# Optimization experiments

Measured on AMD Instinct MI355X. Metric: run time of the kernel, lower is better.

Reference implementation:

```python
import jax
import jax.numpy as jnp
from jax import lax
import numpy as np

INPUT_DIM = 784
HIDDEN_DIM = 1024
BATCH = 256
N_BINS = 10


def setup_inputs() -> dict:
    key = jax.random.key(0)
    k1, k2, k3, k4, k5 = jax.random.split(key, 5)
    # kaiming-normal-ish init scales (faithful in spirit; exact values irrelevant for math)
    W = jax.random.normal(k1, (HIDDEN_DIM, INPUT_DIM), dtype=jnp.float32) * np.sqrt(2.0 / INPUT_DIM)
    c = jnp.zeros((HIDDEN_DIM, 1), dtype=jnp.float32)
    V = jax.random.normal(k2, (INPUT_DIM, HIDDEN_DIM, N_BINS), dtype=jnp.float32) * np.sqrt(2.0 / N_BINS)
    b = jnp.zeros((INPUT_DIM, N_BINS), dtype=jnp.float32)
    x = jax.random.randint(k3, (BATCH, INPUT_DIM), 0, N_BINS, dtype=jnp.int32)
    return {"x": x, "W": W, "c": c, "V": V, "b": b}


def reference(x, W, c, V, b):
    # x: [B, D] int pixel bins; W: [H, D]; c: [H, 1]; V: [D, H, 10]; b: [D, 10]
    B = x.shape[0]
    xf = x.astype(jnp.float32)  # [B, D]
    a0 = jnp.broadcast_to(c[:, 0][None, :], (B, W.shape[0]))  # [B, H]

    def step(a, inp):
        Vi, bi, Wi, xi = inp  # Vi:[H,10], bi:[10], Wi:[H], xi:[B]
        h = jax.nn.sigmoid(a)                       # [B, H]
        p = jax.nn.softmax(h @ Vi + bi, axis=1)     # [B, 10]
        a = a + xi[:, None] * Wi[None, :]           # rank-1 update, matches x_i @ W[:,i].T
        return a, p

    _, p_seq = lax.scan(step, a0, (V, b, W.T, xf.T))  # p_seq: [D, B, 10]
    p_hat = jnp.transpose(p_seq, (1, 2, 0))            # [B, 10, D] == torch.stack(p_hat, dim=2)
    return p_hat
```

## Files before the change

### kernel.cpp

```cpp
#include <hip/hip_runtime.h>
#include <stdint.h>

#define D_DIM 784
#define H_DIM 1024
#define B_DIM 256
#define NBIN  10
#define G_CH  16
#define T_CH  49
#define BT    16
#define LOG2E 1.4426950408889634f

typedef _Float16 half8_t  __attribute__((ext_vector_type(8)));
typedef __fp16   fp16x2_t __attribute__((ext_vector_type(2)));
typedef float    float4_t __attribute__((ext_vector_type(4)));

__global__ void k_transpose(const float* __restrict__ W, float* __restrict__ Wt2) {
    int j = blockIdx.x;
    int t = threadIdx.x;
    int h = t * 4;
    float4 v;
    v.x = W[(size_t)(h+0)*D_DIM + j] * LOG2E;
    v.y = W[(size_t)(h+1)*D_DIM + j] * LOG2E;
    v.z = W[(size_t)(h+2)*D_DIM + j] * LOG2E;
    v.w = W[(size_t)(h+3)*D_DIM + j] * LOG2E;
    ((float4*)(Wt2 + (size_t)j*H_DIM))[t] = v;
}

__global__ void k_vbprep(const float* __restrict__ V, _Float16* __restrict__ VB) {
    int i  = blockIdx.x;
    int kk = blockIdx.y;
    int t  = threadIdx.x;
    int l  = t >> 1;
    int j0 = (t & 1) * 4;
    int n  = l & 15;
    int hbase = kk*32 + (l>>4)*8 + j0;
    union { _Float16 h[4]; uint2 u; } o;
    #pragma unroll
    for (int jj = 0; jj < 4; ++jj) {
        float v = (n < NBIN) ? V[((size_t)i*H_DIM + hbase + jj)*NBIN + n] : 0.0f;
        o.h[jj] = (_Float16)v;
    }
    size_t idx = ((size_t)(i*32 + kk)*64 + l)*8 + j0;
    *((uint2*)(VB + idx)) = o.u;
}

template<typename CT>
__global__ void k_partial(const float* __restrict__ Wt2, const int* __restrict__ x,
                          CT* __restrict__ PA) {
    int tc   = blockIdx.x;
    int hblk = blockIdx.y;
    int bblk = blockIdx.z;
    int t    = threadIdx.x;
    int h    = hblk*256 + t;

    __shared__ __align__(16) float xs[64][G_CH];
    {
        int bl = t >> 2, q = t & 3;
        int4 xi = *((const int4*)(x + (size_t)(bblk*64 + bl)*D_DIM + tc*G_CH + q*4));
        float4 xf = make_float4((float)xi.x, (float)xi.y, (float)xi.z, (float)xi.w);
        *((float4*)&xs[bl][q*4]) = xf;
    }
    float w[G_CH];
    #pragma unroll
    for (int j = 0; j < G_CH; ++j) w[j] = Wt2[(size_t)(tc*G_CH + j)*H_DIM + h];
    __syncthreads();

    for (int bl = 0; bl < 64; ++bl) {
        float acc = 0.0f;
        #pragma unroll
        for (int q = 0; q < 4; ++q) {
            float4 xf = *((float4*)&xs[bl][q*4]);
            acc += xf.x*w[q*4+0] + xf.y*w[q*4+1] + xf.z*w[q*4+2] + xf.w*w[q*4+3];
        }
        PA[((size_t)tc*B_DIM + bblk*64 + bl)*H_DIM + h] = (CT)acc;
    }
}

template<typename CT>
__global__ void k_scan(const float* __restrict__ c, CT* __restrict__ PA) {
    int b = blockIdx.x >> 2;
    int h = (blockIdx.x & 3)*256 + threadIdx.x;
    float acc = c[h] * LOG2E;
    size_t stride = (size_t)B_DIM * H_DIM;
    size_t idx = (size_t)b*H_DIM + h;
    for (int tt = 0; tt < T_CH; ++tt) {
        float v = (float)PA[idx];
        PA[idx] = (CT)acc;
        acc += v;
        idx += stride;
    }
}

template<typename CT>
__global__ __launch_bounds__(256, 3)
void k_main(const float* __restrict__ Wt2, const _Float16* __restrict__ VB,
            const CT* __restrict__ PA, const int* __restrict__ x,
            const float* __restrict__ bias, float* __restrict__ out) {
    int tc  = blockIdx.x;
    int bt  = blockIdx.y;
    int tid = threadIdx.x;
    int w   = tid >> 6;
    int l   = tid & 63;
    int bl  = l & 15;
    int kg  = l >> 4;
    int bg  = bt*BT + bl;
    int i0  = tc*G_CH;

    __shared__ float red[4][256][5];
    __shared__ float bs[G_CH][16];
    __shared__ __align__(16) float plds[BT][NBIN][20];

    {
        int ii = tid >> 4, n = tid & 15;
        bs[ii][n] = (n < NBIN) ? bias[(size_t)(i0+ii)*NBIN + n] : 0.0f;
    }

    float a[8][8];
    {
        const CT* src = PA + ((size_t)tc*B_DIM + bg)*H_DIM + w*256 + kg*8;
        #pragma unroll
        for (int m = 0; m < 8; ++m)
            #pragma unroll
            for (int j = 0; j < 8; ++j)
                a[m][j] = (float)src[m*32 + j];
    }
    __syncthreads();

    const float4* wt4 = (const float4*)Wt2;
    for (int ii = 0; ii < G_CH; ++ii) {
        int i = i0 + ii;
        float xvf = (float)x[(size_t)bg*D_DIM + i];

        uint4 vb[8];
        const uint4* vbp = (const uint4*)VB + ((size_t)i*32 + w*8)*64 + l;
        #pragma unroll
        for (int m = 0; m < 8; ++m) vb[m] = vbp[m*64];

        float4_t cfrag = {0.f, 0.f, 0.f, 0.f};
        #pragma unroll
        for (int m = 0; m < 8; ++m) {
            union { half8_t h8; uint u32[4]; } af;
            #pragma unroll
            for (int p = 0; p < 4; ++p) {
                float s0 = __builtin_amdgcn_rcpf(1.0f + __builtin_amdgcn_exp2f(-a[m][2*p]));
                float s1 = __builtin_amdgcn_rcpf(1.0f + __builtin_amdgcn_exp2f(-a[m][2*p+1]));
                union { fp16x2_t v; uint u; } cv;
                cv.v = __builtin_amdgcn_cvt_pkrtz(s0, s1);
                af.u32[p] = cv.u;
            }
            union { half8_t h8; uint4 u; } bf;
            bf.u = vb[m];
            cfrag = __builtin_amdgcn_mfma_f32_16x16x32_f16(af.h8, bf.h8, cfrag, 0, 0, 0);

            int hb = (w*256 + kg*8 + m*32) >> 2;
            float4 w0 = wt4[(size_t)i*(H_DIM/4) + hb];
            float4 w1 = wt4[(size_t)i*(H_DIM/4) + hb + 1];
            a[m][0] += xvf*w0.x; a[m][1] += xvf*w0.y; a[m][2] += xvf*w0.z; a[m][3] += xvf*w0.w;
            a[m][4] += xvf*w1.x; a[m][5] += xvf*w1.y; a[m][6] += xvf*w1.z; a[m][7] += xvf*w1.w;
        }

        red[w][l][0] = cfrag[0]; red[w][l][1] = cfrag[1];
        red[w][l][2] = cfrag[2]; red[w][l][3] = cfrag[3];
        __syncthreads();
        float tot = red[0][l][w] + red[1][l][w] + red[2][l][w] + red[3][l][w];
        int n = bl;
        float v = (n < NBIN) ? tot + bs[ii][n] : -3.0e38f;
        float vm = v;
        vm = fmaxf(vm, __shfl_xor(vm, 1));
        vm = fmaxf(vm, __shfl_xor(vm, 2));
        vm = fmaxf(vm, __shfl_xor(vm, 4));
        vm = fmaxf(vm, __shfl_xor(vm, 8));
        float e = __builtin_amdgcn_exp2f((v - vm) * LOG2E);
        float ss = e;
        ss += __shfl_xor(ss, 1);
        ss += __shfl_xor(ss, 2);
        ss += __shfl_xor(ss, 4);
        ss += __shfl_xor(ss, 8);
        float p = e * __builtin_amdgcn_rcpf(ss);
        if (n < NBIN) plds[kg*4 + w][n][ii] = p;
        __syncthreads();
    }

    if (tid < BT*NBIN) {
        int bb = tid / NBIN, n = tid % NBIN;
        size_t base = ((size_t)(bt*BT + bb)*NBIN + n)*D_DIM + i0;
        #pragma unroll
        for (int q = 0; q < 4; ++q) {
            float4 v = *((float4*)&plds[bb][n][q*4]);
            *((float4*)(out + base + q*4)) = v;
        }
    }
}

extern "C" void kernel_launch(void* const* d_in, const int* in_sizes, int n_in,
                              void* d_out, int out_size, void* d_ws, size_t ws_size,
                              hipStream_t stream) {
    const int*   x    = (const int*)d_in[0];
    const float* W    = (const float*)d_in[1];
    const float* c    = (const float*)d_in[2];
    const float* V    = (const float*)d_in[3];
    const float* bias = (const float*)d_in[4];
    float* out = (float*)d_out;

    char* ws = (char*)d_ws;
    size_t off = 0;
    float* Wt2 = (float*)(ws + off);
    off += (size_t)D_DIM * H_DIM * sizeof(float);
    off = (off + 255) & ~(size_t)255;
    _Float16* VB = (_Float16*)(ws + off);
    off += (size_t)D_DIM * 32 * 64 * 8 * sizeof(_Float16);
    off = (off + 255) & ~(size_t)255;
    size_t pa_f32 = (size_t)T_CH * B_DIM * H_DIM * sizeof(float);
    bool f32ck = (off + pa_f32) <= ws_size;

    k_transpose<<<dim3(D_DIM), 256, 0, stream>>>(W, Wt2);
    k_vbprep<<<dim3(D_DIM, 32), 128, 0, stream>>>(V, VB);

    if (f32ck) {
        float* PA = (float*)(ws + off);
        k_partial<float><<<dim3(T_CH, 4, 4), 256, 0, stream>>>(Wt2, x, PA);
        k_scan<float><<<dim3(B_DIM * 4), 256, 0, stream>>>(c, PA);
        k_main<float><<<dim3(T_CH, B_DIM / BT), 256, 0, stream>>>(Wt2, VB, PA, x, bias, out);
    } else {
        _Float16* PA = (_Float16*)(ws + off);
        k_partial<_Float16><<<dim3(T_CH, 4, 4), 256, 0, stream>>>(Wt2, x, PA);
        k_scan<_Float16><<<dim3(B_DIM * 4), 256, 0, stream>>>(c, PA);
        k_main<_Float16><<<dim3(T_CH, B_DIM / BT), 256, 0, stream>>>(Wt2, VB, PA, x, bias, out);
    }
}
```

Baseline: 224.4 us.

## Tile transposes, fuse partial+scan kernels, and double-buffer W via LDS in main loop

```diff
diff --git a/kernel.cpp b/kernel.cpp
--- a/kernel.cpp
+++ b/kernel.cpp
@@ -8,6 +8,7 @@
 #define G_CH  16
 #define T_CH  49
 #define BT    16
+#define BF    2
 #define LOG2E 1.4426950408889634f
 
 typedef _Float16 half8_t  __attribute__((ext_vector_type(8)));
@@ -15,79 +16,71 @@
 typedef float    float4_t __attribute__((ext_vector_type(4)));
 
 __global__ void k_transpose(const float* __restrict__ W, float* __restrict__ Wt2) {
-    int j = blockIdx.x;
-    int t = threadIdx.x;
-    int h = t * 4;
-    float4 v;
-    v.x = W[(size_t)(h+0)*D_DIM + j] * LOG2E;
-    v.y = W[(size_t)(h+1)*D_DIM + j] * LOG2E;
-    v.z = W[(size_t)(h+2)*D_DIM + j] * LOG2E;
-    v.w = W[(size_t)(h+3)*D_DIM + j] * LOG2E;
-    ((float4*)(Wt2 + (size_t)j*H_DIM))[t] = v;
+    __shared__ float t[64][65];
+    int j0 = blockIdx.x * 64, h0 = blockIdx.y * 64;
+    int tj = threadIdx.x & 63, tr = threadIdx.x >> 6;
+    int j = j0 + tj;
+    #pragma unroll
+    for (int r = 0; r < 16; ++r) {
+        int hh = tr * 16 + r;
+        t[hh][tj] = (j < D_DIM) ? W[(size_t)(h0 + hh) * D_DIM + j] : 0.0f;
+    }
+    __syncthreads();
+    #pragma unroll
+    for (int r = 0; r < 16; ++r) {
+        int jj = tr * 16 + r;
+        int jo = j0 + jj;
+        if (jo < D_DIM) Wt2[(size_t)jo * H_DIM + h0 + tj] = t[tj][jj] * LOG2E;
+    }
 }
 
 __global__ void k_vbprep(const float* __restrict__ V, _Float16* __restrict__ VB) {
-    int i  = blockIdx.x;
-    int kk = blockIdx.y;
-    int t  = threadIdx.x;
-    int l  = t >> 1;
-    int j0 = (t & 1) * 4;
-    int n  = l & 15;
-    int hbase = kk*32 + (l>>4)*8 + j0;
-    union { _Float16 h[4]; uint2 u; } o;
-    #pragma unroll
-    for (int jj = 0; jj < 4; ++jj) {
-        float v = (n < NBIN) ? V[((size_t)i*H_DIM + hbase + jj)*NBIN + n] : 0.0f;
-        o.h[jj] = (_Float16)v;
-    }
-    size_t idx = ((size_t)(i*32 + kk)*64 + l)*8 + j0;
-    *((uint2*)(VB + idx)) = o.u;
+    int i   = blockIdx.x;
+    int tid = threadIdx.x;
+    __shared__ __align__(16) float vsf[H_DIM * NBIN];
+    const float4* src = (const float4*)(V + (size_t)i * H_DIM * NBIN);
+    #pragma unroll
+    for (int q = 0; q < 10; ++q) {
+        float4 v = src[q * 256 + tid];
+        *((float4*)&vsf[(q * 256 + tid) * 4]) = v;
+    }
+    __syncthreads();
+    #pragma unroll
+    for (int q = 0; q < 8; ++q) {
+        int pair = q * 256 + tid;
+        int kk = pair >> 6, l = pair & 63;
+        int n = l & 15, hb = kk * 32 + ((l >> 4) & 3) * 8;
+        union { _Float16 h[8]; uint4 u; } o;
+        #pragma unroll
+        for (int jj = 0; jj < 8; ++jj)
+            o.h[jj] = (_Float16)((n < NBIN) ? vsf[(hb + jj) * NBIN + n] : 0.0f);
+        ((uint4*)VB)[(size_t)i * 2048 + pair] = o.u;
+    }
 }
 
 template<typename CT>
-__global__ void k_partial(const float* __restrict__ Wt2, const int* __restrict__ x,
-                          CT* __restrict__ PA) {
-    int tc   = blockIdx.x;
-    int hblk = blockIdx.y;
-    int bblk = blockIdx.z;
-    int t    = threadIdx.x;
-    int h    = hblk*256 + t;
-
-    __shared__ __align__(16) float xs[64][G_CH];
-    {
-        int bl = t >> 2, q = t & 3;
-        int4 xi = *((const int4*)(x + (size_t)(bblk*64 + bl)*D_DIM + tc*G_CH + q*4));
+__global__ void k_pscan(const float* __restrict__ Wt2, const int* __restrict__ x,
+                        const float* __restrict__ c, CT* __restrict__ PA) {
+    int b0 = blockIdx.x * BF;
+    int h  = blockIdx.y * 256 + threadIdx.x;
+    __shared__ float xs[BF][D_DIM];
+    for (int q = threadIdx.x; q < BF * (D_DIM / 4); q += 256) {
+        int bb = q / (D_DIM / 4), r = q % (D_DIM / 4);
+        int4 xi = ((const int4*)(x + (size_t)(b0 + bb) * D_DIM))[r];
         float4 xf = make_float4((float)xi.x, (float)xi.y, (float)xi.z, (float)xi.w);
-        *((float4*)&xs[bl][q*4]) = xf;
-    }
-    float w[G_CH];
-    #pragma unroll
-    for (int j = 0; j < G_CH; ++j) w[j] = Wt2[(size_t)(tc*G_CH + j)*H_DIM + h];
-    __syncthreads();
-
-    for (int bl = 0; bl < 64; ++bl) {
-        float acc = 0.0f;
-        #pragma unroll
-        for (int q = 0; q < 4; ++q) {
-            float4 xf = *((float4*)&xs[bl][q*4]);
-            acc += xf.x*w[q*4+0] + xf.y*w[q*4+1] + xf.z*w[q*4+2] + xf.w*w[q*4+3];
-        }
-        PA[((size_t)tc*B_DIM + bblk*64 + bl)*H_DIM + h] = (CT)acc;
-    }
-}
-
-template<typename CT>
-__global__ void k_scan(const float* __restrict__ c, CT* __restrict__ PA) {
-    int b = blockIdx.x >> 2;
-    int h = (blockIdx.x & 3)*256 + threadIdx.x;
-    float acc = c[h] * LOG2E;
-    size_t stride = (size_t)B_DIM * H_DIM;
-    size_t idx = (size_t)b*H_DIM + h;
-    for (int tt = 0; tt < T_CH; ++tt) {
-        float v = (float)PA[idx];
-        PA[idx] = (CT)acc;
-        acc += v;
-        idx += stride;
+        *((float4*)&xs[bb][r * 4]) = xf;
+    }
+    float acc0 = c[h] * LOG2E, acc1 = acc0;
+    __syncthreads();
+    for (int t = 0; t < T_CH; ++t) {
+        PA[((size_t)t * B_DIM + b0 + 0) * H_DIM + h] = (CT)acc0;
+        PA[((size_t)t * B_DIM + b0 + 1) * H_DIM + h] = (CT)acc1;
+        #pragma unroll
+        for (int j = 0; j < G_CH; ++j) {
+            float wv = Wt2[(size_t)(t * G_CH + j) * H_DIM + h];
+            acc0 += xs[0][t * G_CH + j] * wv;
+            acc1 += xs[1][t * G_CH + j] * wv;
+        }
     }
 }
 
@@ -96,54 +89,84 @@
 void k_main(const float* __restrict__ Wt2, const _Float16* __restrict__ VB,
             const CT* __restrict__ PA, const int* __restrict__ x,
             const float* __restrict__ bias, float* __restrict__ out) {
-    int tc  = blockIdx.x;
-    int bt  = blockIdx.y;
+    int bt  = blockIdx.x;
+    int tc  = blockIdx.y;
     int tid = threadIdx.x;
     int w   = tid >> 6;
     int l   = tid & 63;
     int bl  = l & 15;
     int kg  = l >> 4;
-    int bg  = bt*BT + bl;
-    int i0  = tc*G_CH;
+    int bg  = bt * BT + bl;
+    int i0  = tc * G_CH;
 
     __shared__ float red[4][256][5];
     __shared__ float bs[G_CH][16];
     __shared__ __align__(16) float plds[BT][NBIN][20];
+    __shared__ __align__(16) float wlds[2][H_DIM];
 
     {
         int ii = tid >> 4, n = tid & 15;
-        bs[ii][n] = (n < NBIN) ? bias[(size_t)(i0+ii)*NBIN + n] : 0.0f;
-    }
-
+        bs[ii][n] = (n < NBIN) ? bias[(size_t)(i0 + ii) * NBIN + n] : 0.0f;
+    }
+    {
+        float4 wst = *((const float4*)(Wt2 + (size_t)i0 * H_DIM + tid * 4));
+        *((float4*)&wlds[0][tid * 4]) = wst;
+    }
     float a[8][8];
     {
-        const CT* src = PA + ((size_t)tc*B_DIM + bg)*H_DIM + w*256 + kg*8;
+        const CT* src = PA + ((size_t)tc * B_DIM + bg) * H_DIM + w * 256 + kg * 8;
         #pragma unroll
         for (int m = 0; m < 8; ++m)
             #pragma unroll
             for (int j = 0; j < 8; ++j)
-                a[m][j] = (float)src[m*32 + j];
-    }
-    __syncthreads();
-
-    const float4* wt4 = (const float4*)Wt2;
+                a[m][j] = (float)src[m * 32 + j];
+    }
+    int xv = x[(size_t)bg * D_DIM + i0];
+    __syncthreads();
+
+    const uint4* vbbase = (const uint4*)VB;
+    #pragma unroll 2
     for (int ii = 0; ii < G_CH; ++ii) {
         int i = i0 + ii;
-        float xvf = (float)x[(size_t)bg*D_DIM + i];
+        int cur = ii & 1, nxt = cur ^ 1;
 
         uint4 vb[8];
-        const uint4* vbp = (const uint4*)VB + ((size_t)i*32 + w*8)*64 + l;
-        #pragma unroll
-        for (int m = 0; m < 8; ++m) vb[m] = vbp[m*64];
-
+        const uint4* vbp = vbbase + ((size_t)i * 32 + w * 8) * 64 + l;
+        #pragma unroll
+        for (int m = 0; m < 8; ++m) vb[m] = vbp[m * 64];
+        int in2 = (i + 1 < D_DIM) ? i + 1 : i;
+        int xv_n = x[(size_t)bg * D_DIM + in2];
+
+        if (ii > 0) {
+            int ip = ii - 1;
+            float tot = red[0][l][w] + red[1][l][w] + red[2][l][w] + red[3][l][w];
+            int n = bl;
+            float v = (n < NBIN) ? tot + bs[ip][n] : -3.0e38f;
+            float vm = v;
+            vm = fmaxf(vm, __shfl_xor(vm, 1));
+            vm = fmaxf(vm, __shfl_xor(vm, 2));
+            vm = fmaxf(vm, __shfl_xor(vm, 4));
+            vm = fmaxf(vm, __shfl_xor(vm, 8));
+            float e = __builtin_amdgcn_exp2f((v - vm) * LOG2E);
+            float ss = e;
+            ss += __shfl_xor(ss, 1); ss += __shfl_xor(ss, 2);
+            ss += __shfl_xor(ss, 4); ss += __shfl_xor(ss, 8);
+            float p = e * __builtin_amdgcn_rcpf(ss);
+            if (n < NBIN) plds[kg * 4 + w][n][ip] = p;
+        }
+        __syncthreads();
+
+        float4 wst = *((const float4*)(Wt2 + (size_t)in2 * H_DIM + tid * 4));
+
+        float xvf = (float)xv;
         float4_t cfrag = {0.f, 0.f, 0.f, 0.f};
         #pragma unroll
         for (int m = 0; m < 8; ++m) {
             union { half8_t h8; uint u32[4]; } af;
             #pragma unroll
             for (int p = 0; p < 4; ++p) {
-                float s0 = __builtin_amdgcn_rcpf(1.0f + __builtin_amdgcn_exp2f(-a[m][2*p]));
-                float s1 = __builtin_amdgcn_rcpf(1.0f + __builtin_amdgcn_exp2f(-a[m][2*p+1]));
+                float s0 = __builtin_amdgcn_rcpf(1.0f + __builtin_amdgcn_exp2f(-a[m][2 * p]));
+                float s1 = __builtin_amdgcn_rcpf(1.0f + __builtin_amdgcn_exp2f(-a[m][2 * p + 1]));
                 union { fp16x2_t v; uint u; } cv;
                 cv.v = __builtin_amdgcn_cvt_pkrtz(s0, s1);
                 af.u32[p] = cv.u;
@@ -152,19 +175,24 @@
             bf.u = vb[m];
             cfrag = __builtin_amdgcn_mfma_f32_16x16x32_f16(af.h8, bf.h8, cfrag, 0, 0, 0);
 
-            int hb = (w*256 + kg*8 + m*32) >> 2;
-            float4 w0 = wt4[(size_t)i*(H_DIM/4) + hb];
-            float4 w1 = wt4[(size_t)i*(H_DIM/4) + hb + 1];
-            a[m][0] += xvf*w0.x; a[m][1] += xvf*w0.y; a[m][2] += xvf*w0.z; a[m][3] += xvf*w0.w;
-            a[m][4] += xvf*w1.x; a[m][5] += xvf*w1.y; a[m][6] += xvf*w1.z; a[m][7] += xvf*w1.w;
-        }
+            int hb = w * 256 + kg * 8 + m * 32;
+            float4 w0 = *((const float4*)&wlds[cur][hb]);
+            float4 w1 = *((const float4*)&wlds[cur][hb + 4]);
+            a[m][0] += xvf * w0.x; a[m][1] += xvf * w0.y; a[m][2] += xvf * w0.z; a[m][3] += xvf * w0.w;
+            a[m][4] += xvf * w1.x; a[m][5] += xvf * w1.y; a[m][6] += xvf * w1.z; a[m][7] += xvf * w1.w;
+        }
+        *((float4*)&wlds[nxt][tid * 4]) = wst;
+        xv = xv_n;
 
         red[w][l][0] = cfrag[0]; red[w][l][1] = cfrag[1];
         red[w][l][2] = cfrag[2]; red[w][l][3] = cfrag[3];
         __syncthreads();
+    }
+    {
+        int ip = G_CH - 1;
         float tot = red[0][l][w] + red[1][l][w] + red[2][l][w] + red[3][l][w];
         int n = bl;
-        float v = (n < NBIN) ? tot + bs[ii][n] : -3.0e38f;
+        float v = (n < NBIN) ? tot + bs[ip][n] : -3.0e38f;
         float vm = v;
         vm = fmaxf(vm, __shfl_xor(vm, 1));
         vm = fmaxf(vm, __shfl_xor(vm, 2));
@@ -172,22 +200,20 @@
         vm = fmaxf(vm, __shfl_xor(vm, 8));
         float e = __builtin_amdgcn_exp2f((v - vm) * LOG2E);
         float ss = e;
-        ss += __shfl_xor(ss, 1);
-        ss += __shfl_xor(ss, 2);
-        ss += __shfl_xor(ss, 4);
-        ss += __shfl_xor(ss, 8);
+        ss += __shfl_xor(ss, 1); ss += __shfl_xor(ss, 2);
+        ss += __shfl_xor(ss, 4); ss += __shfl_xor(ss, 8);
         float p = e * __builtin_amdgcn_rcpf(ss);
-        if (n < NBIN) plds[kg*4 + w][n][ii] = p;
-        __syncthreads();
-    }
-
-    if (tid < BT*NBIN) {
+        if (n < NBIN) plds[kg * 4 + w][n][ip] = p;
+    }
+    __syncthreads();
+
+    if (tid < BT * NBIN) {
         int bb = tid / NBIN, n = tid % NBIN;
-        size_t base = ((size_t)(bt*BT + bb)*NBIN + n)*D_DIM + i0;
+        size_t base = ((size_t)(bt * BT + bb) * NBIN + n) * D_DIM + i0;
         #pragma unroll
         for (int q = 0; q < 4; ++q) {
-            float4 v = *((float4*)&plds[bb][n][q*4]);
-            *((float4*)(out + base + q*4)) = v;
+            float4 v = *((float4*)&plds[bb][n][q * 4]);
+            *((float4*)(out + base + q * 4)) = v;
         }
     }
 }
@@ -213,18 +239,16 @@
     size_t pa_f32 = (size_t)T_CH * B_DIM * H_DIM * sizeof(float);
     bool f32ck = (off + pa_f32) <= ws_size;
 
-    k_transpose<<<dim3(D_DIM), 256, 0, stream>>>(W, Wt2);
-    k_vbprep<<<dim3(D_DIM, 32), 128, 0, stream>>>(V, VB);
+    k_transpose<<<dim3(13, 16), 256, 0, stream>>>(W, Wt2);
+    k_vbprep<<<dim3(D_DIM), 256, 0, stream>>>(V, VB);
 
     if (f32ck) {
         float* PA = (float*)(ws + off);
-        k_partial<float><<<dim3(T_CH, 4, 4), 256, 0, stream>>>(Wt2, x, PA);
-        k_scan<float><<<dim3(B_DIM * 4), 256, 0, stream>>>(c, PA);
-        k_main<float><<<dim3(T_CH, B_DIM / BT), 256, 0, stream>>>(Wt2, VB, PA, x, bias, out);
+        k_pscan<float><<<dim3(B_DIM / BF, 4), 256, 0, stream>>>(Wt2, x, c, PA);
+        k_main<float><<<dim3(B_DIM / BT, T_CH), 256, 0, stream>>>(Wt2, VB, PA, x, bias, out);
     } else {
         _Float16* PA = (_Float16*)(ws + off);
-        k_partial<_Float16><<<dim3(T_CH, 4, 4), 256, 0, stream>>>(Wt2, x, PA);
-        k_scan<_Float16><<<dim3(B_DIM * 4), 256, 0, stream>>>(c, PA);
-        k_main<_Float16><<<dim3(T_CH, B_DIM / BT), 256, 0, stream>>>(Wt2, VB, PA, x, bias, out);
-    }
-}
+        k_pscan<_Float16><<<dim3(B_DIM / BF, 4), 256, 0, stream>>>(Wt2, x, c, PA);
+        k_main<_Float16><<<dim3(B_DIM / BT, T_CH), 256, 0, stream>>>(Wt2, VB, PA, x, bias, out);
+    }
+}
```

Measured after the change: 251.2 us. +11.9%, slower.
